# Kernel tuning notes

Hardware: AMD Instinct MI355X
Metric: run time of the kernel (lower is better)

The kernel has to match this reference:

```python
import jax, jax.numpy as jnp
from jax import lax
import numpy as np

# NOTE: the original module calls an opaque CUDA 'approximate dot-product' conv kernel.
# Its backward uses EXACT conv2d gradients for input/weight, so the reference forward
# math is the exact conv2d the kernel approximates. `approximate` is a learned scalar
# controlling the hardware approximation level; it does not change the exact-math output.

STRIDE = 1
PAD = (1, 1)  # (padH, padW)


def setup_inputs() -> dict:
    key = jax.random.key(0)
    k1, k2, k3 = jax.random.split(key, 3)
    B, Cin, H, W = 32, 128, 56, 56
    Cout, K = 256, 3
    x = jax.random.normal(k1, (B, Cin, H, W), dtype=jnp.float32)
    # weight init: uniform(-1, 1) per reset_parameters
    weight = jax.random.uniform(k2, (Cout, Cin, K, K), dtype=jnp.float32, minval=-1.0, maxval=1.0)
    fan_in = Cin * K * K
    bound = 1.0 / np.sqrt(fan_in)
    bias = jax.random.uniform(k3, (Cout,), dtype=jnp.float32, minval=-bound, maxval=bound)
    approximate = jnp.ones((1,), dtype=jnp.float32)
    return {"x": x, "weight": weight, "bias": bias, "approximate": approximate}


def reference(x, weight, bias, approximate):
    # Exact conv2d, NCHW input, OIHW kernel. `approximate` controls only the
    # hardware approximation level in the original CUDA kernel.
    out = lax.conv_general_dilated(
        x, weight,
        window_strides=(STRIDE, STRIDE),
        padding=((PAD[0], PAD[0]), (PAD[1], PAD[1])),
        dimension_numbers=("NCHW", "OIHW", "NCHW"),
    )
    return out + bias.reshape(1, -1, 1, 1)
```

## Files before the change

kernel.cpp:

```cpp
#include <hip/hip_runtime.h>


typedef __attribute__((ext_vector_type(8))) short short8;
typedef __attribute__((ext_vector_type(4))) float floatx4;

typedef __attribute__((address_space(1))) const void* gas_ptr;
typedef __attribute__((address_space(3))) void* las_ptr;

__device__ static inline void gl2lds16(const void* g, void* l) {
    __builtin_amdgcn_global_load_lds((gas_ptr)g, (las_ptr)l, 16, 0, 0);
}

__device__ static inline float bf2f(unsigned short u) {
    union { unsigned int i; float f; } x; x.i = ((unsigned int)u) << 16; return x.f;
}
__device__ static inline unsigned short f2bf(float f) {
    union { float f; unsigned int i; } x; x.f = f;
    unsigned int r = (x.i + 0x7FFFu + ((x.i >> 16) & 1u)) >> 16;
    return (unsigned short)r;
}

__device__ static inline bool wave_detect_bf16(const unsigned int* __restrict__ p) {
    const int lane = threadIdx.x & 63;
    int cnt = 0;
#pragma unroll
    for (int r = 0; r < 4; ++r) {
        unsigned int w = p[r * 64 + lane];
        unsigned short lo = (unsigned short)(w & 0xFFFFu);
        int e = (lo >> 7) & 0xFF;
        bool plaus = (lo == 0) || (e >= 96 && e <= 144);
        cnt += (int)__popcll(__ballot(plaus));
    }
    return cnt >= 205;
}

__global__ void wt_repack(const void* __restrict__ wsrc,
                          unsigned short* __restrict__ wt) {
    const bool isbf = wave_detect_bf16((const unsigned int*)wsrc);
    int idx = blockIdx.x * 256 + threadIdx.x;
    int ci  = idx & 127;
    int co  = (idx >> 7) & 255;
    int off = idx >> 15;
    size_t s = (size_t)(co * 128 + ci) * 9 + off;
    float v = isbf ? bf2f(((const unsigned short*)wsrc)[s])
                   : ((const float*)wsrc)[s];
    wt[idx] = f2bf(v);
}

__global__ __launch_bounds__(256) void x_repack(
    const void* __restrict__ xsrc, unsigned short* __restrict__ xp) {
    __shared__ unsigned short tile[56 * 130];
    const int bh  = blockIdx.x;
    const int b   = bh / 58, hp = bh - b * 58;
    const int tid = threadIdx.x;
    unsigned short* row = xp + (size_t)(b * 58 + hp) * 58 * 128;
    if (hp == 0 || hp == 57) {
        uint4 z; z.x = z.y = z.z = z.w = 0u;
        uint4* r = (uint4*)row;
        for (int t = tid; t < 928; t += 256) r[t] = z;
        return;
    }
    const bool isbf = wave_detect_bf16((const unsigned int*)xsrc);
    const int h = hp - 1;
    if (isbf) {
        const unsigned short* xs =
            (const unsigned short*)xsrc + (size_t)b * 128 * 3136 + h * 56;
#pragma unroll
        for (int it = 0; it < 7; ++it) {
            int idx = it * 256 + tid;
            int ci = idx / 14, w4 = idx - ci * 14;
            ushort4 v = *(const ushort4*)(xs + (size_t)ci * 3136 + w4 * 4);
            tile[(w4 * 4 + 0) * 130 + ci] = v.x;
            tile[(w4 * 4 + 1) * 130 + ci] = v.y;
            tile[(w4 * 4 + 2) * 130 + ci] = v.z;
            tile[(w4 * 4 + 3) * 130 + ci] = v.w;
        }
    } else {
        const float* xs = (const float*)xsrc + (size_t)b * 128 * 3136 + h * 56;
#pragma unroll
        for (int it = 0; it < 7; ++it) {
            int idx = it * 256 + tid;
            int ci = idx / 14, w4 = idx - ci * 14;
            float4 v = *(const float4*)(xs + (size_t)ci * 3136 + w4 * 4);
            tile[(w4 * 4 + 0) * 130 + ci] = f2bf(v.x);
            tile[(w4 * 4 + 1) * 130 + ci] = f2bf(v.y);
            tile[(w4 * 4 + 2) * 130 + ci] = f2bf(v.z);
            tile[(w4 * 4 + 3) * 130 + ci] = f2bf(v.w);
        }
    }
    __syncthreads();
#pragma unroll
    for (int it = 0; it < 4; ++it) {
        int k = it * 256 + tid;
        if (k >= 928) break;
        int wq = k >> 4, cc = k & 15;
        uint4 v;
        if (wq == 0 || wq == 57) { v.x = v.y = v.z = v.w = 0u; }
        else {
            const unsigned short* p = &tile[(wq - 1) * 130 + cc * 8];
            union { unsigned short s[8]; uint4 u; } pk;
#pragma unroll
            for (int j = 0; j < 8; ++j) pk.s[j] = p[j];
            v = pk.u;
        }
        *(uint4*)(row + wq * 128 + cc * 8) = v;
    }
}

__global__ __launch_bounds__(512, 2) void conv_mfma(
    const unsigned short* __restrict__ xp,
    const unsigned short* __restrict__ wt,
    const void* __restrict__ bias,
    void* __restrict__ out,
    const void* __restrict__ xorig)
{
    __shared__ __align__(16) char lds[131072];
    const int tid   = threadIdx.x;
    const int lane  = tid & 63;
    const int wv    = tid >> 6;
    const int ntile = blockIdx.x;

    const bool isbf = wave_detect_bf16((const unsigned int*)xorig);

    const bool isA = (wv < 4);
    const int  clg = (lane & 3) ^ ((lane >> 3) & 3);
    const int  rsub = lane >> 2;
    unsigned sb[4]; int db[4];
    if (isA) {
#pragma unroll
        for (int s = 0; s < 4; ++s) {
            const int c  = (wv & 3) * 4 + s;
            const int co = c * 16 + rsub;
            sb[s] = (unsigned)(co * 256 + clg * 16);
            db[s] = c * 1024;
        }
    } else {
#pragma unroll
        for (int s = 0; s < 4; ++s) {
            const int c = (wv & 3) * 4 + s;
            const int n = ntile * 256 + c * 16 + rsub;
            const int b = n / 3136, rem = n - b * 3136;
            const int hh = rem / 56, ww = rem - hh * 56;
            sb[s] = (unsigned)((((b * 58 + hh) * 58 + ww) * 256) + clg * 16);
            db[s] = 16384 + c * 1024;
        }
    }
    const char* gbase = isA ? (const char*)wt : (const char*)xp;

    auto hdelta = [&](int h) -> int {
        const int off = h >> 2, q = h & 3;
        if (isA) return off * 65536 + q * 64;
        const int dh = off / 3, dw = off - dh * 3;
        return (dh * 58 + dw) * 256 + q * 64;
    };

    const int fr = lane & 15;
    const int ph = (lane >> 4) ^ ((fr >> 1) & 3);
    const int wm = wv >> 2;
    const int wn = wv & 3;
    const int aOff = (wm * 128 + fr) * 64 + ph * 16;
    const int bOff = 16384 + (wn * 64 + fr) * 64 + ph * 16;

    floatx4 acc[8][4] = {};

#pragma unroll
    for (int h = 0; h < 3; ++h) {
        char* lb = lds + (h & 3) * 32768;
        const int d = hdelta(h);
#pragma unroll
        for (int s = 0; s < 4; ++s)
            gl2lds16(gbase + sb[s] + d, lb + db[s]);
    }
    __builtin_amdgcn_s_waitcnt(0x3F78);
    __builtin_amdgcn_s_barrier();

#pragma unroll 4
    for (int h = 0; h < 36; ++h) {
        const char* la  = lds + (h & 3) * 32768;
        char* sdst      = lds + ((h + 3) & 3) * 32768;
        const int  dlt  = (h < 33) ? hdelta(h + 3) : 0;
        short8 af[8], bf[4];

#pragma unroll
        for (int i = 0; i < 4; ++i)
            af[i] = *(const short8*)(la + aOff + i * 1024);
#pragma unroll
        for (int j = 0; j < 4; ++j)
            bf[j] = *(const short8*)(la + bOff + j * 1024);
        if (h < 33) {
            gl2lds16(gbase + sb[0] + dlt, sdst + db[0]);
            gl2lds16(gbase + sb[1] + dlt, sdst + db[1]);
        }
        __builtin_amdgcn_s_barrier();
        __builtin_amdgcn_s_setprio(1);
#pragma unroll
        for (int i = 0; i < 4; ++i)
#pragma unroll
            for (int j = 0; j < 4; ++j)
                acc[i][j] = __builtin_amdgcn_mfma_f32_16x16x32_bf16(
                    af[i], bf[j], acc[i][j], 0, 0, 0);
        __builtin_amdgcn_s_setprio(0);
        __builtin_amdgcn_s_barrier();

#pragma unroll
        for (int i = 0; i < 4; ++i)
            af[4 + i] = *(const short8*)(la + aOff + (4 + i) * 1024);
        if (h < 33) {
            gl2lds16(gbase + sb[2] + dlt, sdst + db[2]);
            gl2lds16(gbase + sb[3] + dlt, sdst + db[3]);
        }
        __builtin_amdgcn_s_barrier();
        __builtin_amdgcn_s_setprio(1);
#pragma unroll
        for (int i = 0; i < 4; ++i)
#pragma unroll
            for (int j = 0; j < 4; ++j)
                acc[4 + i][j] = __builtin_amdgcn_mfma_f32_16x16x32_bf16(
                    af[4 + i], bf[j], acc[4 + i][j], 0, 0, 0);
        __builtin_amdgcn_s_setprio(0);

        if (h < 35) {
            if (h <= 32)      __builtin_amdgcn_s_waitcnt(0x3F78);
            else if (h == 33) __builtin_amdgcn_s_waitcnt(0x3F74);
            else              __builtin_amdgcn_s_waitcnt(0x3F70);
            __builtin_amdgcn_s_barrier();
        }
    }

    const int q4 = (lane >> 4) << 2;
    int nb[4], ns[4];
#pragma unroll
    for (int j = 0; j < 4; ++j) {
        const int n = ntile * 256 + wn * 64 + j * 16 + fr;
        nb[j] = n / 3136;
        ns[j] = n - nb[j] * 3136;
    }
#pragma unroll
    for (int i = 0; i < 8; ++i) {
        const int co = wm * 128 + i * 16 + q4;
        float bv[4];
        if (isbf) {
            const ushort4 bb = *(const ushort4*)((const unsigned short*)bias + co);
            bv[0] = bf2f(bb.x); bv[1] = bf2f(bb.y);
            bv[2] = bf2f(bb.z); bv[3] = bf2f(bb.w);
        } else {
            const float4 bb = *(const float4*)((const float*)bias + co);
            bv[0] = bb.x; bv[1] = bb.y; bv[2] = bb.z; bv[3] = bb.w;
        }
#pragma unroll
        for (int j = 0; j < 4; ++j) {
#pragma unroll
            for (int r = 0; r < 4; ++r) {
                const float v = acc[i][j][r] + bv[r];
                const size_t o = (size_t)nb[j] * 802816 +
                                 (size_t)(co + r) * 3136 + ns[j];
                if (isbf) ((unsigned short*)out)[o] = f2bf(v);
                else      ((float*)out)[o] = v;
            }
        }
    }
}

__global__ void conv_naive(const float* __restrict__ x,
                           const float* __restrict__ w,
                           const float* __restrict__ bias,
                           float* __restrict__ out) {
    long long i = (long long)blockIdx.x * 256 + threadIdx.x;
    if (i >= 25690112LL) return;
    int wo = (int)(i % 56); long long t = i / 56;
    int ho = (int)(t % 56); t /= 56;
    int co = (int)(t % 256); int b = (int)(t / 256);
    float acc = bias[co];
    for (int ci = 0; ci < 128; ++ci)
        for (int dh = 0; dh < 3; ++dh) {
            int hi = ho + dh - 1; if ((unsigned)hi >= 56u) continue;
            for (int dw = 0; dw < 3; ++dw) {
                int wi = wo + dw - 1; if ((unsigned)wi >= 56u) continue;
                acc += x[((size_t)(b * 128 + ci) * 56 + hi) * 56 + wi] *
                       w[((co * 128 + ci) * 3 + dh) * 3 + dw];
            }
        }
    out[i] = acc;
}

extern "C" void kernel_launch(void* const* d_in, const int* in_sizes, int n_in,
                              void* d_out, int out_size, void* d_ws, size_t ws_size,
                              hipStream_t stream) {
    const void* x    = d_in[0];
    const void* w    = d_in[1];
    const void* bias = d_in[2];

    const size_t xp_bytes = (size_t)32 * 58 * 58 * 128 * 2;
    const size_t wt_off   = xp_bytes;
    const size_t wt_bytes = (size_t)9 * 256 * 128 * 2;
    const size_t need     = wt_off + wt_bytes;

    if (ws_size >= need) {
        unsigned short* xp = (unsigned short*)d_ws;
        unsigned short* wt = (unsigned short*)((char*)d_ws + wt_off);
        x_repack<<<32 * 58, 256, 0, stream>>>(x, xp);
        wt_repack<<<1152, 256, 0, stream>>>(w, wt);
        conv_mfma<<<dim3(392, 1, 1), 512, 0, stream>>>(xp, wt, bias, d_out, x);
    } else {
        conv_naive<<<(25690112 + 255) / 256, 256, 0, stream>>>(
            (const float*)x, (const float*)w, (const float*)bias, (float*)d_out);
    }
}
```

Before: 216.9 us.

## Use 4 waves with 128x128 warp tiles and double-buffered LDS

Halves the block to 256 threads, with each wave computing a 128x128 output tile (8x8 MFMA accumulators) instead of 128x64. Every wave now loads both A and B slices. The LDS pipeline goes from a 4-stage ring with split-phase barriers to a simple 2-stage double buffer with one barrier per K step. The aim is more LDS fragment reuse per MFMA and fewer barriers. The cost is 256 accumulator VGPRs per lane, which risks spills or lower occupancy, plus a shallower prefetch depth.

```diff
diff --git a/kernel.cpp b/kernel.cpp
--- a/kernel.cpp
+++ b/kernel.cpp
@@ -107,14 +107,14 @@
     }
 }
 
-__global__ __launch_bounds__(512, 2) void conv_mfma(
+__global__ __launch_bounds__(256, 2) void conv_mfma(
     const unsigned short* __restrict__ xp,
     const unsigned short* __restrict__ wt,
     const void* __restrict__ bias,
     void* __restrict__ out,
     const void* __restrict__ xorig)
 {
-    __shared__ __align__(16) char lds[131072];
+    __shared__ __align__(16) char lds[65536];
     const int tid   = threadIdx.x;
     const int lane  = tid & 63;
     const int wv    = tid >> 6;
@@ -122,116 +122,84 @@
 
     const bool isbf = wave_detect_bf16((const unsigned int*)xorig);
 
-    const bool isA = (wv < 4);
-    const int  clg = (lane & 3) ^ ((lane >> 3) & 3);
-    const int  rsub = lane >> 2;
-    unsigned sb[4]; int db[4];
-    if (isA) {
-#pragma unroll
-        for (int s = 0; s < 4; ++s) {
-            const int c  = (wv & 3) * 4 + s;
-            const int co = c * 16 + rsub;
-            sb[s] = (unsigned)(co * 256 + clg * 16);
-            db[s] = c * 1024;
-        }
-    } else {
-#pragma unroll
-        for (int s = 0; s < 4; ++s) {
-            const int c = (wv & 3) * 4 + s;
-            const int n = ntile * 256 + c * 16 + rsub;
-            const int b = n / 3136, rem = n - b * 3136;
-            const int hh = rem / 56, ww = rem - hh * 56;
-            sb[s] = (unsigned)((((b * 58 + hh) * 58 + ww) * 256) + clg * 16);
-            db[s] = 16384 + c * 1024;
-        }
-    }
-    const char* gbase = isA ? (const char*)wt : (const char*)xp;
-
-    auto hdelta = [&](int h) -> int {
-        const int off = h >> 2, q = h & 3;
-        if (isA) return off * 65536 + q * 64;
-        const int dh = off / 3, dw = off - dh * 3;
-        return (dh * 58 + dw) * 256 + q * 64;
-    };
+    const int clg  = (lane & 3) ^ ((lane >> 3) & 3);
+    const int rsub = lane >> 2;
+    unsigned sbA[4], sbB[4];
+    int dbA[4], dbB[4];
+#pragma unroll
+    for (int s = 0; s < 4; ++s) {
+        const int c  = wv * 4 + s;
+        const int co = c * 16 + rsub;
+        sbA[s] = (unsigned)(co * 256 + clg * 16);
+        dbA[s] = c * 1024;
+        const int n = ntile * 256 + c * 16 + rsub;
+        const int b = n / 3136, rem = n - b * 3136;
+        const int hh = rem / 56, ww = rem - hh * 56;
+        sbB[s] = (unsigned)(((b * 58 + hh) * 58 + ww) * 256 + clg * 16);
+        dbB[s] = 16384 + c * 1024;
+    }
 
     const int fr = lane & 15;
     const int ph = (lane >> 4) ^ ((fr >> 1) & 3);
-    const int wm = wv >> 2;
-    const int wn = wv & 3;
+    const int wm = wv >> 1;
+    const int wn = wv & 1;
     const int aOff = (wm * 128 + fr) * 64 + ph * 16;
-    const int bOff = 16384 + (wn * 64 + fr) * 64 + ph * 16;
-
-    floatx4 acc[8][4] = {};
-
-#pragma unroll
-    for (int h = 0; h < 3; ++h) {
-        char* lb = lds + (h & 3) * 32768;
-        const int d = hdelta(h);
-#pragma unroll
-        for (int s = 0; s < 4; ++s)
-            gl2lds16(gbase + sb[s] + d, lb + db[s]);
-    }
-    __builtin_amdgcn_s_waitcnt(0x3F78);
+    const int bOff = 16384 + (wn * 128 + fr) * 64 + ph * 16;
+
+    floatx4 acc[8][8] = {};
+
+#pragma unroll
+    for (int s = 0; s < 4; ++s)
+        gl2lds16((const char*)wt + sbA[s], lds + dbA[s]);
+#pragma unroll
+    for (int s = 0; s < 4; ++s)
+        gl2lds16((const char*)xp + sbB[s], lds + dbB[s]);
+    __builtin_amdgcn_s_waitcnt(0x3F70);
     __builtin_amdgcn_s_barrier();
 
-#pragma unroll 4
+#pragma unroll 2
     for (int h = 0; h < 36; ++h) {
-        const char* la  = lds + (h & 3) * 32768;
-        char* sdst      = lds + ((h + 3) & 3) * 32768;
-        const int  dlt  = (h < 33) ? hdelta(h + 3) : 0;
-        short8 af[8], bf[4];
-
-#pragma unroll
-        for (int i = 0; i < 4; ++i)
+        const char* la = lds + (h & 1) * 32768;
+        if (h < 35) {
+            char* sd = lds + ((h + 1) & 1) * 32768;
+            const int hn  = h + 1;
+            const int off = hn >> 2, q = hn & 3;
+            const int dA  = off * 65536 + q * 64;
+            const int dh_ = off / 3, dw_ = off - dh_ * 3;
+            const int dB  = (dh_ * 58 + dw_) * 256 + q * 64;
+#pragma unroll
+            for (int s = 0; s < 4; ++s)
+                gl2lds16((const char*)wt + sbA[s] + dA, sd + dbA[s]);
+#pragma unroll
+            for (int s = 0; s < 4; ++s)
+                gl2lds16((const char*)xp + sbB[s] + dB, sd + dbB[s]);
+        }
+        short8 af[8], bf[8];
+#pragma unroll
+        for (int i = 0; i < 8; ++i)
             af[i] = *(const short8*)(la + aOff + i * 1024);
 #pragma unroll
-        for (int j = 0; j < 4; ++j)
+        for (int j = 0; j < 8; ++j)
             bf[j] = *(const short8*)(la + bOff + j * 1024);
-        if (h < 33) {
-            gl2lds16(gbase + sb[0] + dlt, sdst + db[0]);
-            gl2lds16(gbase + sb[1] + dlt, sdst + db[1]);
-        }
-        __builtin_amdgcn_s_barrier();
         __builtin_amdgcn_s_setprio(1);
 #pragma unroll
-        for (int i = 0; i < 4; ++i)
-#pragma unroll
-            for (int j = 0; j < 4; ++j)
+        for (int i = 0; i < 8; ++i)
+#pragma unroll
+            for (int j = 0; j < 8; ++j)
                 acc[i][j] = __builtin_amdgcn_mfma_f32_16x16x32_bf16(
                     af[i], bf[j], acc[i][j], 0, 0, 0);
         __builtin_amdgcn_s_setprio(0);
-        __builtin_amdgcn_s_barrier();
-
-#pragma unroll
-        for (int i = 0; i < 4; ++i)
-            af[4 + i] = *(const short8*)(la + aOff + (4 + i) * 1024);
-        if (h < 33) {
-            gl2lds16(gbase + sb[2] + dlt, sdst + db[2]);
-            gl2lds16(gbase + sb[3] + dlt, sdst + db[3]);
-        }
-        __builtin_amdgcn_s_barrier();
-        __builtin_amdgcn_s_setprio(1);
-#pragma unroll
-        for (int i = 0; i < 4; ++i)
-#pragma unroll
-            for (int j = 0; j < 4; ++j)
-                acc[4 + i][j] = __builtin_amdgcn_mfma_f32_16x16x32_bf16(
-                    af[4 + i], bf[j], acc[4 + i][j], 0, 0, 0);
-        __builtin_amdgcn_s_setprio(0);
-
         if (h < 35) {
-            if (h <= 32)      __builtin_amdgcn_s_waitcnt(0x3F78);
-            else if (h == 33) __builtin_amdgcn_s_waitcnt(0x3F74);
-            else              __builtin_amdgcn_s_waitcnt(0x3F70);
+            __builtin_amdgcn_s_waitcnt(0x3F70);
             __builtin_amdgcn_s_barrier();
         }
     }
 
     const int q4 = (lane >> 4) << 2;
-    int nb[4], ns[4];
-#pragma unroll
-    for (int j = 0; j < 4; ++j) {
-        const int n = ntile * 256 + wn * 64 + j * 16 + fr;
+    int nb[8], ns[8];
+#pragma unroll
+    for (int j = 0; j < 8; ++j) {
+        const int n = ntile * 256 + wn * 128 + j * 16 + fr;
         nb[j] = n / 3136;
         ns[j] = n - nb[j] * 3136;
     }
@@ -248,7 +216,7 @@
             bv[0] = bb.x; bv[1] = bb.y; bv[2] = bb.z; bv[3] = bb.w;
         }
 #pragma unroll
-        for (int j = 0; j < 4; ++j) {
+        for (int j = 0; j < 8; ++j) {
 #pragma unroll
             for (int r = 0; r < 4; ++r) {
                 const float v = acc[i][j][r] + bv[r];
@@ -300,7 +268,7 @@
         unsigned short* wt = (unsigned short*)((char*)d_ws + wt_off);
         x_repack<<<32 * 58, 256, 0, stream>>>(x, xp);
         wt_repack<<<1152, 256, 0, stream>>>(w, wt);
-        conv_mfma<<<dim3(392, 1, 1), 512, 0, stream>>>(xp, wt, bias, d_out, x);
+        conv_mfma<<<dim3(392, 1, 1), 256, 0, stream>>>(xp, wt, bias, d_out, x);
     } else {
         conv_naive<<<(25690112 + 255) / 256, 256, 0, stream>>>(
             (const float*)x, (const float*)w, (const float*)bias, (float*)d_out);
```

After: 599.2 us. 2.76x slower.
